# Optimization experiments

Measured on AMD Instinct MI355X. Metric: run time of the kernel, lower is better.

Reference implementation:

```python
import jax, jax.numpy as jnp
import numpy as np

N = 50000          # nodes
E = 1600000        # edges (avg degree 32)
D_IN = 128
D_OUT = 128
NEG_SLOPE = 0.01   # F.leaky_relu default (module ignores its negative_slope attr)


def setup_inputs() -> dict:
    key = jax.random.key(0)
    k = jax.random.split(key, 7)
    h = jax.random.normal(k[0], (N, D_IN), dtype=jnp.float32)
    embedding = jax.random.normal(k[1], (N, D_OUT), dtype=jnp.float32)
    # params (xavier-ish scaling)
    W_lin = jax.random.normal(k[2], (D_OUT, D_IN), dtype=jnp.float32) * (2.0 / (D_IN + D_OUT)) ** 0.5
    w_fc = jax.random.normal(k[3], (1, 2 * D_OUT), dtype=jnp.float32) * (2.0 / (2 * D_OUT + 1)) ** 0.5
    w_emb = jax.random.normal(k[4], (1, 2 * D_OUT), dtype=jnp.float32) * (2.0 / (2 * D_OUT + 1)) ** 0.5
    src = jax.random.randint(k[5], (E,), 0, N, dtype=jnp.int64 if jax.config.jax_enable_x64 else jnp.int32)
    dst = jax.random.randint(k[6], (E,), 0, N, dtype=jnp.int64 if jax.config.jax_enable_x64 else jnp.int32)
    return {"h": h, "embedding": embedding, "W_lin": W_lin, "w_fc": w_fc,
            "w_emb": w_emb, "src": src, "dst": dst}


def reference(h, embedding, W_lin, w_fc, w_emb, src, dst):
    n = h.shape[0]
    d = W_lin.shape[0]
    # z = lin(h): [N, out]
    z = h @ W_lin.T
    # attn_fc(cat(z_src, z_dst)) + attn_embed(cat(e_src, e_dst)) split into per-node
    # scalar scores so we gather [E] scalars instead of materializing [E, 2*out].
    s_fc_src = z @ w_fc[0, :d]            # [N]
    s_fc_dst = z @ w_fc[0, d:]            # [N]
    s_em_src = embedding @ w_emb[0, :d]   # [N]
    s_em_dst = embedding @ w_emb[0, d:]   # [N]
    a = (s_fc_src + s_em_src)[src] + (s_fc_dst + s_em_dst)[dst]   # [E]
    e = jnp.where(a > 0, a, NEG_SLOPE * a)  # leaky_relu, slope 0.01
    # segment softmax over incoming edges of each dst node
    m = jax.ops.segment_max(e, dst, num_segments=n)               # [N]
    e_exp = jnp.exp(e - m[dst])                                   # [E]
    denom = jax.ops.segment_sum(e_exp, dst, num_segments=n)       # [N]
    alpha = e_exp / denom[dst]                                    # [E]
    # weighted neighbor aggregation: h_out[v] = sum_{(u->v)} alpha * z[u]
    h_out = jax.ops.segment_sum(alpha[:, None] * z[src], dst, num_segments=n)
    return h_out
```

## Files before the change

kernel.cpp:

```cpp
#include <hip/hip_runtime.h>
#include <hip/hip_bf16.h>

#define D 128
#define BSH 7
#define BDST 128
#define NCHK 256
#define CAPB 5120
#define SL 8

typedef __attribute__((ext_vector_type(8))) short short8;
typedef __attribute__((ext_vector_type(4))) float f32x4;

__device__ __forceinline__ unsigned short f2bf(float f) {
  unsigned u = __float_as_uint(f);
  unsigned r = (u + 0x7FFFu + ((u >> 16) & 1u)) >> 16;
  return (unsigned short)r;
}

__global__ __launch_bounds__(256) void k_wconv(const float* __restrict__ W,
                                               unsigned short* __restrict__ Wb) {
  const int i = blockIdx.x * 256 + threadIdx.x;
  float4 f = ((const float4*)W)[i];
  ushort4 o;
  o.x = f2bf(f.x); o.y = f2bf(f.y); o.z = f2bf(f.z); o.w = f2bf(f.w);
  ((ushort4*)Wb)[i] = o;
}

__global__ __launch_bounds__(256) void k_lin(const float* __restrict__ h,
                                             const unsigned short* __restrict__ Wb,
                                             const float* __restrict__ w_fc,
                                             const float* __restrict__ emb,
                                             const float* __restrict__ w_emb,
                                             unsigned* __restrict__ zd,
                                             float* __restrict__ a_src,
                                             float* __restrict__ a_dst, int n) {
  __shared__ float sfs[4][16], sfd[4][16];
  const int lane = threadIdx.x & 63;
  const int wid = threadIdx.x >> 6;
  const int m0 = blockIdx.x * 64 + wid * 16;
  if (m0 >= n) return;
  const int c = lane & 15;
  const int g = lane >> 4;

  int arow = m0 + c;
  if (arow >= n) arow = n - 1;
  const float4* hrow = (const float4*)(h + (size_t)arow * 128);

  short8 afr[4];
#pragma unroll
  for (int s = 0; s < 4; ++s) {
    float4 f0 = hrow[8 * s + 2 * g];
    float4 f1 = hrow[8 * s + 2 * g + 1];
    short8 a;
    a[0] = (short)f2bf(f0.x); a[1] = (short)f2bf(f0.y);
    a[2] = (short)f2bf(f0.z); a[3] = (short)f2bf(f0.w);
    a[4] = (short)f2bf(f1.x); a[5] = (short)f2bf(f1.y);
    a[6] = (short)f2bf(f1.z); a[7] = (short)f2bf(f1.w);
    afr[s] = a;
  }

  f32x4 acc[8];
#pragma unroll
  for (int t = 0; t < 8; ++t) acc[t] = (f32x4){0.f, 0.f, 0.f, 0.f};

#pragma unroll
  for (int s = 0; s < 4; ++s) {
#pragma unroll
    for (int t = 0; t < 8; ++t) {
      short8 b = *(const short8*)(Wb + ((size_t)(t * 16 + c) * 128 + 32 * s + 8 * g));
      acc[t] = __builtin_amdgcn_mfma_f32_16x16x32_bf16(afr[s], b, acc[t], 0, 0, 0);
    }
  }

  float wfs[8], wfd[8];
#pragma unroll
  for (int t = 0; t < 8; ++t) {
    wfs[t] = w_fc[t * 16 + c];
    wfd[t] = w_fc[128 + t * 16 + c];
  }

  const int rbase = m0 + 4 * g;
#pragma unroll
  for (int r = 0; r < 4; ++r) {
    const int row = rbase + r;
    if (row < n) {
#pragma unroll
      for (int tp = 0; tp < 4; ++tp) {
        unsigned dw = ((unsigned)f2bf(acc[tp + 4][r]) << 16) | (unsigned)f2bf(acc[tp][r]);
        zd[(size_t)row * 64 + tp * 16 + c] = dw;
      }
    }
    float ps = 0.f, pd = 0.f;
#pragma unroll
    for (int t = 0; t < 8; ++t) {
      ps += acc[t][r] * wfs[t];
      pd += acc[t][r] * wfd[t];
    }
#pragma unroll
    for (int off = 1; off < 16; off <<= 1) {
      ps += __shfl_xor(ps, off, 64);
      pd += __shfl_xor(pd, off, 64);
    }
    if (c == 0) {
      sfs[wid][4 * g + r] = ps;
      sfd[wid][4 * g + r] = pd;
    }
  }
  __syncthreads();

  const int nloc = lane >> 2;
  const int qc = lane & 3;
  const int node2 = m0 + nloc;
  float es = 0.f, ed = 0.f;
  if (node2 < n) {
    const float4* er = (const float4*)(emb + (size_t)node2 * 128 + qc * 32);
    const float4* wsp = (const float4*)(w_emb + qc * 32);
    const float4* wdp = (const float4*)(w_emb + 128 + qc * 32);
#pragma unroll
    for (int j = 0; j < 8; ++j) {
      float4 e4 = er[j], s4 = wsp[j], d4 = wdp[j];
      es += e4.x * s4.x + e4.y * s4.y + e4.z * s4.z + e4.w * s4.w;
      ed += e4.x * d4.x + e4.y * d4.y + e4.z * d4.z + e4.w * d4.w;
    }
  }
  es += __shfl_xor(es, 1, 64); es += __shfl_xor(es, 2, 64);
  ed += __shfl_xor(ed, 1, 64); ed += __shfl_xor(ed, 2, 64);
  if (qc == 0 && node2 < n) {
    a_src[node2] = es + sfs[wid][nloc];
    a_dst[node2] = ed + sfd[wid][nloc];
  }
}

__global__ __launch_bounds__(256) void k_hscat(const int* __restrict__ src,
                                               const int* __restrict__ dst,
                                               int* __restrict__ bincur,
                                               unsigned* __restrict__ binrec,
                                               int E, int NB, int CHSZ) {
  __shared__ int hl[512];
  __shared__ int cur[512];
  const int tid = threadIdx.x, c = blockIdx.x;
  for (int i = tid; i < NB; i += 256) hl[i] = 0;
  __syncthreads();
  const int beg = c * CHSZ, end = min(beg + CHSZ, E);
  for (int i = beg + tid; i < end; i += 256) atomicAdd(&hl[dst[i] >> BSH], 1);
  __syncthreads();
  for (int b = tid; b < NB; b += 256) {
    int cb = hl[b];
    cur[b] = cb > 0 ? atomicAdd(&bincur[b], cb) : 0;
  }
  __syncthreads();
  for (int i = beg + tid; i < end; i += 256) {
    int d = dst[i];
    int b = d >> BSH;
    int pos = atomicAdd(&cur[b], 1);
    binrec[(size_t)b * CAPB + pos] =
        ((unsigned)src[i] << BSH) | (unsigned)(d & (BDST - 1));
  }
}

__global__ __launch_bounds__(256) void k_build(const unsigned* __restrict__ binrec,
                                               const int* __restrict__ bincur,
                                               int2* __restrict__ row2,
                                               int* __restrict__ csr, int n) {
  __shared__ int hist[BDST * SL];
  __shared__ int excl[BDST * SL];
  __shared__ int sh[256];
  const int tid = threadIdx.x, b = blockIdx.x;
  const int cntb = bincur[b];
  const unsigned* rb = binrec + (size_t)b * CAPB;
  const int base = b * CAPB;

  for (int k = tid; k < BDST * SL; k += 256) hist[k] = 0;
  __syncthreads();
  for (int i = tid; i < cntb; i += 256) {
    unsigned r = rb[i];
    int dl = r & (BDST - 1);
    int sv = (int)(r >> BSH);
    atomicAdd(&hist[dl * SL + (sv >> 13)], 1);
  }
  __syncthreads();
  const int k0 = tid * 4;
  int v4[4], s = 0;
#pragma unroll
  for (int j = 0; j < 4; ++j) { v4[j] = hist[k0 + j]; s += v4[j]; }
  sh[tid] = s;
  __syncthreads();
  for (int off = 1; off < 256; off <<= 1) {
    int a = (tid >= off) ? sh[tid - off] : 0;
    __syncthreads();
    sh[tid] += a;
    __syncthreads();
  }
  int e0 = sh[tid] - s;
#pragma unroll
  for (int j = 0; j < 4; ++j) { excl[k0 + j] = e0; e0 += v4[j]; }
  __syncthreads();
  if (tid < BDST) {
    int bg = excl[tid * SL];
    int en = (tid == BDST - 1) ? cntb : excl[(tid + 1) * SL];
    int v = b * BDST + tid;
    if (v < n) row2[v] = make_int2(base + bg, base + en);
  }
  __syncthreads();
  for (int i = tid; i < cntb; i += 256) {
    unsigned r = rb[i];
    int dl = r & (BDST - 1);
    int sv = (int)(r >> BSH);
    int pos = base + atomicAdd(&excl[dl * SL + (sv >> 13)], 1);
    csr[pos] = sv;
  }
}

__global__ __launch_bounds__(256) void k_agg(const unsigned* __restrict__ zd,
                                             const float* __restrict__ a_src,
                                             const float* __restrict__ a_dst,
                                             const int2* __restrict__ row2,
                                             const int* __restrict__ csr,
                                             float* __restrict__ out, int n) {
  const int lane = threadIdx.x & 63;
  const int grp = lane >> 4;
  const int sub = lane & 15;
  const int v = blockIdx.x * 4 + (threadIdx.x >> 6);
  if (v >= n) return;
  const int2 be = row2[v];
  const int beg = be.x, end = be.y;
  const float adv = a_dst[v];

  float accf[8];
#pragma unroll
  for (int j = 0; j < 8; ++j) accf[j] = 0.f;
  float ews = 0.f;

#pragma unroll 4
  for (int i = beg + grp; i < end; i += 4) {
    const int u = csr[i];
    const float a = a_src[u] + adv;
    const float e = a > 0.f ? a : 0.01f * a;
    const float ew = __expf(e);
    const uint4 zz = ((const uint4*)zd)[(size_t)u * 16 + sub];
    ews += ew;
    accf[0] += ew * __uint_as_float(zz.x << 16);
    accf[1] += ew * __uint_as_float(zz.x & 0xffff0000u);
    accf[2] += ew * __uint_as_float(zz.y << 16);
    accf[3] += ew * __uint_as_float(zz.y & 0xffff0000u);
    accf[4] += ew * __uint_as_float(zz.z << 16);
    accf[5] += ew * __uint_as_float(zz.z & 0xffff0000u);
    accf[6] += ew * __uint_as_float(zz.w << 16);
    accf[7] += ew * __uint_as_float(zz.w & 0xffff0000u);
  }

#pragma unroll
  for (int off = 16; off <= 32; off <<= 1) {
    ews += __shfl_xor(ews, off, 64);
#pragma unroll
    for (int j = 0; j < 8; ++j) accf[j] += __shfl_xor(accf[j], off, 64);
  }

  if (grp == 0) {
    const float inv = (end > beg) ? 1.f / ews : 0.f;
    float4 olo = make_float4(accf[0] * inv, accf[2] * inv, accf[4] * inv, accf[6] * inv);
    float4 ohi = make_float4(accf[1] * inv, accf[3] * inv, accf[5] * inv, accf[7] * inv);
    ((float4*)out)[(size_t)v * 32 + sub] = olo;
    ((float4*)out)[(size_t)v * 32 + 16 + sub] = ohi;
  }
}

extern "C" void kernel_launch(void* const* d_in, const int* in_sizes, int n_in,
                              void* d_out, int out_size, void* d_ws, size_t ws_size,
                              hipStream_t stream) {
  const float* h = (const float*)d_in[0];
  const float* emb = (const float*)d_in[1];
  const float* W = (const float*)d_in[2];
  const float* wfc = (const float*)d_in[3];
  const float* wemb = (const float*)d_in[4];
  const int* src = (const int*)d_in[5];
  const int* dst = (const int*)d_in[6];
  const int n = in_sizes[0] / D;
  const int E = in_sizes[5];
  const int NB = (n + BDST - 1) >> BSH;
  const int CHSZ = (E + NCHK - 1) / NCHK;

  char* ws = (char*)d_ws;
  size_t off = 0;
  auto alloc = [&](size_t bytes) {
    void* p = ws + off;
    off = (off + bytes + 255) & ~(size_t)255;
    return p;
  };
  unsigned* zd = (unsigned*)alloc((size_t)n * 64 * 4);
  unsigned short* Wb = (unsigned short*)alloc(D * D * 2);
  float* a_src = (float*)alloc((size_t)n * 4);
  float* a_dst = (float*)alloc((size_t)n * 4);
  int* bincur = (int*)alloc((size_t)NB * 4);
  int2* row2 = (int2*)alloc((size_t)n * 8);
  unsigned* binrec = (unsigned*)alloc((size_t)NB * CAPB * 4);
  int* csr = (int*)alloc((size_t)NB * CAPB * 4);
  (void)off;
  (void)ws_size;

  (void)hipMemsetAsync(bincur, 0, (size_t)NB * 4, stream);
  k_wconv<<<(D * D / 4 + 255) / 256, 256, 0, stream>>>(W, Wb);
  k_lin<<<(n + 63) / 64, 256, 0, stream>>>(h, Wb, wfc, emb, wemb, zd, a_src, a_dst, n);
  k_hscat<<<NCHK, 256, 0, stream>>>(src, dst, bincur, binrec, E, NB, CHSZ);
  k_build<<<NB, 256, 0, stream>>>(binrec, bincur, row2, csr, n);
  k_agg<<<(n + 3) / 4, 256, 0, stream>>>(zd, a_src, a_dst, row2, csr, (float*)d_out, n);
}
```

Measured before the change: 138.6 us.

## Merge linear projection and edge binning into one launch; pack aggregation accumulators

Folds the independent k_lin and k_hscat kernels into a single horizontally fused launch: the first NCHK blocks do edge binning and the remaining blocks do the bf16 linear projection and score computation. This removes one kernel launch and lets the two independent workloads share the GPU concurrently. Separately, the aggregation accumulators are recast as float2 vectors, which may let the compiler emit packed FMA instructions. Shared memory per block now covers both roles, which could lower occupancy for the linear part.

Measured after the change: 124.7 us. 10.1% less time.

```diff
diff --git a/kernel.cpp b/kernel.cpp
--- a/kernel.cpp
+++ b/kernel.cpp
@@ -10,6 +10,7 @@
 
 typedef __attribute__((ext_vector_type(8))) short short8;
 typedef __attribute__((ext_vector_type(4))) float f32x4;
+typedef __attribute__((ext_vector_type(2))) float f32x2;
 
 __device__ __forceinline__ unsigned short f2bf(float f) {
   unsigned u = __float_as_uint(f);
@@ -26,18 +27,44 @@
   ((ushort4*)Wb)[i] = o;
 }
 
-__global__ __launch_bounds__(256) void k_lin(const float* __restrict__ h,
-                                             const unsigned short* __restrict__ Wb,
-                                             const float* __restrict__ w_fc,
-                                             const float* __restrict__ emb,
-                                             const float* __restrict__ w_emb,
-                                             unsigned* __restrict__ zd,
-                                             float* __restrict__ a_src,
-                                             float* __restrict__ a_dst, int n) {
+__global__ __launch_bounds__(256) void k_combo(
+    const float* __restrict__ h, const unsigned short* __restrict__ Wb,
+    const float* __restrict__ w_fc, const float* __restrict__ emb,
+    const float* __restrict__ w_emb, unsigned* __restrict__ zd,
+    float* __restrict__ a_src, float* __restrict__ a_dst,
+    const int* __restrict__ src, const int* __restrict__ dst,
+    int* __restrict__ bincur, unsigned* __restrict__ binrec,
+    int n, int E, int NB, int CHSZ) {
+  __shared__ int hl[512];
+  __shared__ int cur[512];
   __shared__ float sfs[4][16], sfd[4][16];
-  const int lane = threadIdx.x & 63;
-  const int wid = threadIdx.x >> 6;
-  const int m0 = blockIdx.x * 64 + wid * 16;
+  const int tid = threadIdx.x;
+
+  if ((int)blockIdx.x < NCHK) {
+    const int c = blockIdx.x;
+    for (int i = tid; i < NB; i += 256) hl[i] = 0;
+    __syncthreads();
+    const int beg = c * CHSZ, end = min(beg + CHSZ, E);
+    for (int i = beg + tid; i < end; i += 256) atomicAdd(&hl[dst[i] >> BSH], 1);
+    __syncthreads();
+    for (int b = tid; b < NB; b += 256) {
+      int cb = hl[b];
+      cur[b] = cb > 0 ? atomicAdd(&bincur[b], cb) : 0;
+    }
+    __syncthreads();
+    for (int i = beg + tid; i < end; i += 256) {
+      int d = dst[i];
+      int b = d >> BSH;
+      int pos = atomicAdd(&cur[b], 1);
+      binrec[(size_t)b * CAPB + pos] =
+          ((unsigned)src[i] << BSH) | (unsigned)(d & (BDST - 1));
+    }
+    return;
+  }
+
+  const int lane = tid & 63;
+  const int wid = tid >> 6;
+  const int m0 = (blockIdx.x - NCHK) * 64 + wid * 16;
   if (m0 >= n) return;
   const int c = lane & 15;
   const int g = lane >> 4;
@@ -128,33 +155,6 @@
   if (qc == 0 && node2 < n) {
     a_src[node2] = es + sfs[wid][nloc];
     a_dst[node2] = ed + sfd[wid][nloc];
-  }
-}
-
-__global__ __launch_bounds__(256) void k_hscat(const int* __restrict__ src,
-                                               const int* __restrict__ dst,
-                                               int* __restrict__ bincur,
-                                               unsigned* __restrict__ binrec,
-                                               int E, int NB, int CHSZ) {
-  __shared__ int hl[512];
-  __shared__ int cur[512];
-  const int tid = threadIdx.x, c = blockIdx.x;
-  for (int i = tid; i < NB; i += 256) hl[i] = 0;
-  __syncthreads();
-  const int beg = c * CHSZ, end = min(beg + CHSZ, E);
-  for (int i = beg + tid; i < end; i += 256) atomicAdd(&hl[dst[i] >> BSH], 1);
-  __syncthreads();
-  for (int b = tid; b < NB; b += 256) {
-    int cb = hl[b];
-    cur[b] = cb > 0 ? atomicAdd(&bincur[b], cb) : 0;
-  }
-  __syncthreads();
-  for (int i = beg + tid; i < end; i += 256) {
-    int d = dst[i];
-    int b = d >> BSH;
-    int pos = atomicAdd(&cur[b], 1);
-    binrec[(size_t)b * CAPB + pos] =
-        ((unsigned)src[i] << BSH) | (unsigned)(d & (BDST - 1));
   }
 }
 
@@ -226,9 +226,9 @@
   const int beg = be.x, end = be.y;
   const float adv = a_dst[v];
 
-  float accf[8];
-#pragma unroll
-  for (int j = 0; j < 8; ++j) accf[j] = 0.f;
+  f32x2 acc2[4];
+#pragma unroll
+  for (int j = 0; j < 4; ++j) acc2[j] = (f32x2){0.f, 0.f};
   float ews = 0.f;
 
 #pragma unroll 4
@@ -239,27 +239,31 @@
     const float ew = __expf(e);
     const uint4 zz = ((const uint4*)zd)[(size_t)u * 16 + sub];
     ews += ew;
-    accf[0] += ew * __uint_as_float(zz.x << 16);
-    accf[1] += ew * __uint_as_float(zz.x & 0xffff0000u);
-    accf[2] += ew * __uint_as_float(zz.y << 16);
-    accf[3] += ew * __uint_as_float(zz.y & 0xffff0000u);
-    accf[4] += ew * __uint_as_float(zz.z << 16);
-    accf[5] += ew * __uint_as_float(zz.z & 0xffff0000u);
-    accf[6] += ew * __uint_as_float(zz.w << 16);
-    accf[7] += ew * __uint_as_float(zz.w & 0xffff0000u);
+    const f32x2 ew2 = {ew, ew};
+    f32x2 z0 = {__uint_as_float(zz.x << 16), __uint_as_float(zz.x & 0xffff0000u)};
+    f32x2 z1 = {__uint_as_float(zz.y << 16), __uint_as_float(zz.y & 0xffff0000u)};
+    f32x2 z2 = {__uint_as_float(zz.z << 16), __uint_as_float(zz.z & 0xffff0000u)};
+    f32x2 z3 = {__uint_as_float(zz.w << 16), __uint_as_float(zz.w & 0xffff0000u)};
+    acc2[0] += ew2 * z0;
+    acc2[1] += ew2 * z1;
+    acc2[2] += ew2 * z2;
+    acc2[3] += ew2 * z3;
   }
 
 #pragma unroll
   for (int off = 16; off <= 32; off <<= 1) {
     ews += __shfl_xor(ews, off, 64);
 #pragma unroll
-    for (int j = 0; j < 8; ++j) accf[j] += __shfl_xor(accf[j], off, 64);
+    for (int j = 0; j < 4; ++j) {
+      acc2[j][0] += __shfl_xor(acc2[j][0], off, 64);
+      acc2[j][1] += __shfl_xor(acc2[j][1], off, 64);
+    }
   }
 
   if (grp == 0) {
     const float inv = (end > beg) ? 1.f / ews : 0.f;
-    float4 olo = make_float4(accf[0] * inv, accf[2] * inv, accf[4] * inv, accf[6] * inv);
-    float4 ohi = make_float4(accf[1] * inv, accf[3] * inv, accf[5] * inv, accf[7] * inv);
+    float4 olo = make_float4(acc2[0][0] * inv, acc2[1][0] * inv, acc2[2][0] * inv, acc2[3][0] * inv);
+    float4 ohi = make_float4(acc2[0][1] * inv, acc2[1][1] * inv, acc2[2][1] * inv, acc2[3][1] * inv);
     ((float4*)out)[(size_t)v * 32 + sub] = olo;
     ((float4*)out)[(size_t)v * 32 + 16 + sub] = ohi;
   }
@@ -279,6 +283,7 @@
   const int E = in_sizes[5];
   const int NB = (n + BDST - 1) >> BSH;
   const int CHSZ = (E + NCHK - 1) / NCHK;
+  const int NLIN = (n + 63) / 64;
 
   char* ws = (char*)d_ws;
   size_t off = 0;
@@ -300,8 +305,8 @@
 
   (void)hipMemsetAsync(bincur, 0, (size_t)NB * 4, stream);
   k_wconv<<<(D * D / 4 + 255) / 256, 256, 0, stream>>>(W, Wb);
-  k_lin<<<(n + 63) / 64, 256, 0, stream>>>(h, Wb, wfc, emb, wemb, zd, a_src, a_dst, n);
-  k_hscat<<<NCHK, 256, 0, stream>>>(src, dst, bincur, binrec, E, NB, CHSZ);
+  k_combo<<<NCHK + NLIN, 256, 0, stream>>>(h, Wb, wfc, emb, wemb, zd, a_src, a_dst,
+                                           src, dst, bincur, binrec, n, E, NB, CHSZ);
   k_build<<<NB, 256, 0, stream>>>(binrec, bincur, row2, csr, n);
   k_agg<<<(n + 3) / 4, 256, 0, stream>>>(zd, a_src, a_dst, row2, csr, (float*)d_out, n);
 }
```
